# Kernel tuning notes

Hardware: AMD Instinct MI355X
Metric: run time of the kernel (lower is better)

Reference implementation:

```python
import jax, jax.numpy as jnp
import numpy as np
import math

DIM_PER_HEAD = 64

def setup_inputs() -> dict:
    key = jax.random.key(0)
    k1, k2, k3, k4 = jax.random.split(key, 4)
    B, H, S, D = 2, 16, 2048, 64
    mat1 = jax.random.normal(k1, (B, H, S, D), dtype=jnp.float32)
    mat2 = jax.random.normal(k2, (B, H, S, D), dtype=jnp.float32)
    mat3 = jax.random.normal(k3, (B, H, S, D), dtype=jnp.float32)
    bias = jax.random.normal(k4, (1, 1, S, S), dtype=jnp.float32)
    return {"mat1": mat1, "mat2": mat2, "mat3": mat3, "bias": bias}

def reference(mat1, mat2, mat3, bias) -> jnp.ndarray:
    # scale Q, scores = QK^T + bias, softmax over last dim, then @ V
    scale = 1.0 / math.sqrt(DIM_PER_HEAD)
    qk = jnp.einsum('bhqd,bhkd->bhqk', mat1 * scale, mat2)  # [B,H,S,S]
    scores = jax.nn.softmax(qk + bias, axis=-1)
    return jnp.einsum('bhqk,bhkd->bhqd', scores, mat3)
```

## Files before the change

### kernel.cpp

```cpp
#include <hip/hip_runtime.h>
#include <hip/hip_bf16.h>


#define SEQ 2048
#define DH  64
#define BHN 32
#define LOG2E 1.44269504088896f

typedef __attribute__((ext_vector_type(8))) short bf16x8;
typedef __attribute__((ext_vector_type(4))) float f32x4;
typedef __attribute__((ext_vector_type(8))) short short8v;

__device__ inline short f2b(float x) {
    union { float f; unsigned u; } v; v.f = x;
    unsigned r = v.u + 0x7fff + ((v.u >> 16) & 1);
    return (short)(r >> 16);
}

__device__ inline void gl_lds16(const void* g, void* l) {
    __builtin_amdgcn_global_load_lds(
        (const __attribute__((address_space(1))) void*)g,
        (__attribute__((address_space(3))) void*)l, 16, 0, 0);
}

__global__ __launch_bounds__(256)
void prep_kv(const float* __restrict__ K, const float* __restrict__ V,
             short* __restrict__ Kb, short* __restrict__ Vt) {
    __shared__ short t[64 * 72];
    const int tid = threadIdx.x;
    const int bh = blockIdx.x >> 5, st = blockIdx.x & 31, s0 = st * 64;

    {
        const float* Kp = K + ((size_t)bh * SEQ + s0) * DH;
        short* Ko = Kb + ((size_t)bh * SEQ + s0) * DH;
        #pragma unroll
        for (int i = 0; i < 2; ++i) {
            size_t o = (size_t)(tid + i * 256) * 8;
            f32x4 a = *(const f32x4*)(Kp + o);
            f32x4 b = *(const f32x4*)(Kp + o + 4);
            short8v s;
            #pragma unroll
            for (int j = 0; j < 4; ++j) { s[j] = f2b(a[j]); s[4 + j] = f2b(b[j]); }
            *(short8v*)(Ko + o) = s;
        }
    }

    const float* Vb = V + (size_t)bh * SEQ * DH + (size_t)s0 * DH;
    #pragma unroll
    for (int i = 0; i < 4; ++i) {
        int c = tid + i * 256, s = c >> 4, c4 = c & 15;
        f32x4 v = *(const f32x4*)(Vb + s * DH + c4 * 4);
        #pragma unroll
        for (int j = 0; j < 4; ++j) t[s * 72 + c4 * 4 + j] = f2b(v[j]);
    }
    __syncthreads();
    const int d = tid >> 2, part = tid & 3;
    short8v lo, hi;
    #pragma unroll
    for (int j = 0; j < 8; ++j) {
        lo[j] = t[(part * 16 + j) * 72 + d];
        hi[j] = t[(part * 16 + 8 + j) * 72 + d];
    }
    short* outp = Vt + (size_t)bh * DH * SEQ + (size_t)d * SEQ + s0 + part * 16;
    *(short8v*)outp = lo;
    *(short8v*)(outp + 8) = hi;
}

__global__ __launch_bounds__(256, 4)
void mha_main(const float* __restrict__ Q, const float* __restrict__ Bias,
              const short* __restrict__ Kb, const short* __restrict__ Vt,
              float* __restrict__ Out)
{
    __shared__ short lds_k[64 * DH];
    __shared__ short lds_v[DH * 64];
    __shared__ short lds_p[4 * 16 * 64];

    const int tid = threadIdx.x, lane = tid & 63, wave = tid >> 6;
    const int l15 = lane & 15, l4 = lane >> 4;
    const int qb = blockIdx.x & 31, bh = blockIdx.x >> 5;
    const int q0 = qb * 64;

    const float* Qb = Q + (size_t)bh * SEQ * DH;
    const short* Kh = Kb + (size_t)bh * SEQ * DH;
    const short* Vh = Vt + (size_t)bh * DH * SEQ;
    float* Ob = Out + (size_t)bh * SEQ * DH;

    bf16x8 qf[2];
    {
        const float* qp = Qb + (size_t)(q0 + wave * 16 + l15) * DH;
        #pragma unroll
        for (int ks = 0; ks < 2; ++ks) {
            short tmp[8];
            #pragma unroll
            for (int j = 0; j < 8; ++j) tmp[j] = f2b(qp[ks * 32 + l4 * 8 + j] * 0.125f);
            qf[ks] = *reinterpret_cast<bf16x8*>(tmp);
        }
    }

    f32x4 o_acc[4];
    #pragma unroll
    for (int dt = 0; dt < 4; ++dt) o_acc[dt] = f32x4{0.f, 0.f, 0.f, 0.f};
    float l_part[4] = {0.f, 0.f, 0.f, 0.f};

    const short* kg[2]; const short* vg[2]; short* kl[2]; short* vl[2];
    #pragma unroll
    for (int p = 0; p < 2; ++p) {
        int slot = p * 256 + wave * 64 + lane;
        int r_ = slot >> 3;
        int c_ = slot & 7;
        int cg = c_ ^ (r_ & 7);
        kg[p] = Kh + (size_t)r_ * DH + cg * 8;
        vg[p] = Vh + (size_t)r_ * SEQ + cg * 8;
        kl[p] = &lds_k[(size_t)(p * 256 + wave * 64) * 8];
        vl[p] = &lds_v[(size_t)(p * 256 + wave * 64) * 8];
    }
    const float* bp0 = Bias + (size_t)(q0 + wave * 16 + l4 * 4) * SEQ + l15;
    short* pw = &lds_p[wave * 16 * 64];
    const int swz = l15 & 7;

    for (int kt = 0; kt < SEQ / 64; ++kt) {
        const int k0 = kt * 64;
        __syncthreads();
        gl_lds16(kg[0] + (size_t)k0 * DH, kl[0]);
        gl_lds16(kg[1] + (size_t)k0 * DH, kl[1]);
        gl_lds16(vg[0] + k0, vl[0]);
        gl_lds16(vg[1] + k0, vl[1]);

        f32x4 sacc[4];
        const float* bp = bp0 + k0;
        #pragma unroll
        for (int nt = 0; nt < 4; ++nt)
            #pragma unroll
            for (int r = 0; r < 4; ++r)
                sacc[nt][r] = bp[(size_t)r * SEQ + nt * 16];

        __syncthreads();

        #pragma unroll
        for (int ks = 0; ks < 2; ++ks)
            #pragma unroll
            for (int nt = 0; nt < 4; ++nt) {
                int cc = (ks * 4 + l4) ^ swz;
                bf16x8 kf = *(const bf16x8*)&lds_k[(nt * 16 + l15) * DH + cc * 8];
                sacc[nt] = __builtin_amdgcn_mfma_f32_16x16x32_bf16(qf[ks], kf, sacc[nt], 0, 0, 0);
            }

        #pragma unroll
        for (int r = 0; r < 4; ++r) {
            const int prow = l4 * 4 + r;
            const int rsw = prow & 7;
            #pragma unroll
            for (int nt = 0; nt < 4; ++nt) {
                float pv = __builtin_amdgcn_exp2f(sacc[nt][r] * LOG2E);
                l_part[r] += pv;
                int pc = (nt * 2 + (l15 >> 3)) ^ rsw;
                pw[prow * 64 + pc * 8 + (l15 & 7)] = f2b(pv);
            }
        }

        #pragma unroll
        for (int ks = 0; ks < 2; ++ks) {
            int cc = (ks * 4 + l4) ^ swz;
            bf16x8 pf = *(const bf16x8*)&pw[l15 * 64 + cc * 8];
            #pragma unroll
            for (int dt = 0; dt < 4; ++dt) {
                bf16x8 vf = *(const bf16x8*)&lds_v[(dt * 16 + l15) * DH + cc * 8];
                o_acc[dt] = __builtin_amdgcn_mfma_f32_16x16x32_bf16(pf, vf, o_acc[dt], 0, 0, 0);
            }
        }
    }

    #pragma unroll
    for (int r = 0; r < 4; ++r) {
        float s = l_part[r];
        #pragma unroll
        for (int m = 1; m < 16; m <<= 1) s += __shfl_xor(s, m, 64);
        l_part[r] = s;
    }

    #pragma unroll
    for (int r = 0; r < 4; ++r) {
        float inv = 1.0f / l_part[r];
        float* op = Ob + (size_t)(q0 + wave * 16 + l4 * 4 + r) * DH + l15;
        #pragma unroll
        for (int dt = 0; dt < 4; ++dt) op[dt * 16] = o_acc[dt][r] * inv;
    }
}

extern "C" void kernel_launch(void* const* d_in, const int* in_sizes, int n_in,
                              void* d_out, int out_size, void* d_ws, size_t ws_size,
                              hipStream_t stream) {
    const float* Q    = (const float*)d_in[0];
    const float* K    = (const float*)d_in[1];
    const float* V    = (const float*)d_in[2];
    const float* Bias = (const float*)d_in[3];
    float* O          = (float*)d_out;

    short* Kb = (short*)d_ws;
    short* Vt = Kb + (size_t)BHN * SEQ * DH;

    prep_kv<<<dim3(BHN * 32), dim3(256), 0, stream>>>(K, V, Kb, Vt);
    mha_main<<<dim3(BHN * 32), dim3(256), 0, stream>>>(Q, Bias, Kb, Vt, O);
}
```

Measured before the change: 168.6 us.

## Double-buffer K/V tiles in LDS and prefetch bias one tile ahead

The K/V shared-memory tiles become two buffers, so the global-to-LDS load of tile kt+1 is issued while tile kt is being computed. The bias values for the next tile are also prefetched into registers. This cuts the loop to one barrier per iteration and hides global load latency behind the MFMA and exp work. LOG2E is folded into the Q scale and the bias, which removes a multiply from the exp path. In exchange, LDS use roughly doubles and register pressure rises, which could reduce occupancy.

```diff
diff --git a/kernel.cpp b/kernel.cpp
--- a/kernel.cpp
+++ b/kernel.cpp
@@ -5,6 +5,7 @@
 #define SEQ 2048
 #define DH  64
 #define BHN 32
+#define NTILE (SEQ / 64)
 #define LOG2E 1.44269504088896f
 
 typedef __attribute__((ext_vector_type(8))) short bf16x8;
@@ -71,8 +72,8 @@
               const short* __restrict__ Kb, const short* __restrict__ Vt,
               float* __restrict__ Out)
 {
-    __shared__ short lds_k[64 * DH];
-    __shared__ short lds_v[DH * 64];
+    __shared__ short lds_k[2][64 * DH];
+    __shared__ short lds_v[2][64 * DH];
     __shared__ short lds_p[4 * 16 * 64];
 
     const int tid = threadIdx.x, lane = tid & 63, wave = tid >> 6;
@@ -88,11 +89,12 @@
     bf16x8 qf[2];
     {
         const float* qp = Qb + (size_t)(q0 + wave * 16 + l15) * DH;
+        const float qs = 0.125f * LOG2E;
         #pragma unroll
         for (int ks = 0; ks < 2; ++ks) {
             short tmp[8];
             #pragma unroll
-            for (int j = 0; j < 8; ++j) tmp[j] = f2b(qp[ks * 32 + l4 * 8 + j] * 0.125f);
+            for (int j = 0; j < 8; ++j) tmp[j] = f2b(qp[ks * 32 + l4 * 8 + j] * qs);
             qf[ks] = *reinterpret_cast<bf16x8*>(tmp);
         }
     }
@@ -111,37 +113,66 @@
         int cg = c_ ^ (r_ & 7);
         kg[p] = Kh + (size_t)r_ * DH + cg * 8;
         vg[p] = Vh + (size_t)r_ * SEQ + cg * 8;
-        kl[p] = &lds_k[(size_t)(p * 256 + wave * 64) * 8];
-        vl[p] = &lds_v[(size_t)(p * 256 + wave * 64) * 8];
+        kl[p] = &lds_k[0][(size_t)(p * 256 + wave * 64) * 8];
+        vl[p] = &lds_v[0][(size_t)(p * 256 + wave * 64) * 8];
     }
     const float* bp0 = Bias + (size_t)(q0 + wave * 16 + l4 * 4) * SEQ + l15;
     short* pw = &lds_p[wave * 16 * 64];
     const int swz = l15 & 7;
 
-    for (int kt = 0; kt < SEQ / 64; ++kt) {
-        const int k0 = kt * 64;
-        __syncthreads();
-        gl_lds16(kg[0] + (size_t)k0 * DH, kl[0]);
-        gl_lds16(kg[1] + (size_t)k0 * DH, kl[1]);
-        gl_lds16(vg[0] + k0, vl[0]);
-        gl_lds16(vg[1] + k0, vl[1]);
+    gl_lds16(kg[0], kl[0]);
+    gl_lds16(kg[1], kl[1]);
+    gl_lds16(vg[0], vl[0]);
+    gl_lds16(vg[1], vl[1]);
+
+    float bpre[4][4];
+    #pragma unroll
+    for (int nt = 0; nt < 4; ++nt)
+        #pragma unroll
+        for (int r = 0; r < 4; ++r)
+            bpre[nt][r] = bp0[(size_t)r * SEQ + nt * 16];
+
+    __syncthreads();
+
+    for (int kt = 0; kt < NTILE; ++kt) {
+        const int cur = kt & 1;
+        const int nb = cur ^ 1;
+
+        if (kt + 1 < NTILE) {
+            const size_t koff = (size_t)(kt + 1) * 64 * DH;
+            const int voff = (kt + 1) * 64;
+            const int lo = nb * (64 * DH);
+            gl_lds16(kg[0] + koff, kl[0] + lo);
+            gl_lds16(kg[1] + koff, kl[1] + lo);
+            gl_lds16(vg[0] + voff, vl[0] + lo);
+            gl_lds16(vg[1] + voff, vl[1] + lo);
+        }
 
         f32x4 sacc[4];
-        const float* bp = bp0 + k0;
         #pragma unroll
         for (int nt = 0; nt < 4; ++nt)
             #pragma unroll
             for (int r = 0; r < 4; ++r)
-                sacc[nt][r] = bp[(size_t)r * SEQ + nt * 16];
-
-        __syncthreads();
+                sacc[nt][r] = bpre[nt][r] * LOG2E;
+
+        if (kt + 1 < NTILE) {
+            const float* bp = bp0 + (kt + 1) * 64;
+            #pragma unroll
+            for (int nt = 0; nt < 4; ++nt)
+                #pragma unroll
+                for (int r = 0; r < 4; ++r)
+                    bpre[nt][r] = bp[(size_t)r * SEQ + nt * 16];
+        }
+
+        const short* lk = lds_k[cur];
+        const short* lv = lds_v[cur];
 
         #pragma unroll
         for (int ks = 0; ks < 2; ++ks)
             #pragma unroll
             for (int nt = 0; nt < 4; ++nt) {
                 int cc = (ks * 4 + l4) ^ swz;
-                bf16x8 kf = *(const bf16x8*)&lds_k[(nt * 16 + l15) * DH + cc * 8];
+                bf16x8 kf = *(const bf16x8*)&lk[(nt * 16 + l15) * DH + cc * 8];
                 sacc[nt] = __builtin_amdgcn_mfma_f32_16x16x32_bf16(qf[ks], kf, sacc[nt], 0, 0, 0);
             }
 
@@ -151,7 +182,7 @@
             const int rsw = prow & 7;
             #pragma unroll
             for (int nt = 0; nt < 4; ++nt) {
-                float pv = __builtin_amdgcn_exp2f(sacc[nt][r] * LOG2E);
+                float pv = __builtin_amdgcn_exp2f(sacc[nt][r]);
                 l_part[r] += pv;
                 int pc = (nt * 2 + (l15 >> 3)) ^ rsw;
                 pw[prow * 64 + pc * 8 + (l15 & 7)] = f2b(pv);
@@ -164,10 +195,12 @@
             bf16x8 pf = *(const bf16x8*)&pw[l15 * 64 + cc * 8];
             #pragma unroll
             for (int dt = 0; dt < 4; ++dt) {
-                bf16x8 vf = *(const bf16x8*)&lds_v[(dt * 16 + l15) * DH + cc * 8];
+                bf16x8 vf = *(const bf16x8*)&lv[(dt * 16 + l15) * DH + cc * 8];
                 o_acc[dt] = __builtin_amdgcn_mfma_f32_16x16x32_bf16(pf, vf, o_acc[dt], 0, 0, 0);
             }
         }
+
+        __syncthreads();
     }
 
     #pragma unroll
```

Result: no change. 169.4 us (+0.5%).

## Keep softmax probabilities in registers via transposed MFMA and permlane swaps

Applied to the files above, without the earlier changes.

Swaps the MFMA operand order so S^T is computed, giving each lane a row's contiguous keys. The bias can then be read as float4 vectors and the P tile repacked into the PV A-operand with packed bf16 converts and permlane16/32 swaps, which drops the LDS round trip for P. LOG2E is folded into the Q scale and the bias, and the row-sum reduction becomes two shuffles plus a broadcast. It uses gfx950-specific instructions, and the correctness of the lane permutation depends on the MFMA register layout.

```diff
diff --git a/kernel.cpp b/kernel.cpp
--- a/kernel.cpp
+++ b/kernel.cpp
@@ -5,6 +5,7 @@
 #define SEQ 2048
 #define DH  64
 #define BHN 32
+#define NTILE (SEQ / 64)
 #define LOG2E 1.44269504088896f
 
 typedef __attribute__((ext_vector_type(8))) short bf16x8;
@@ -15,6 +16,19 @@
     union { float f; unsigned u; } v; v.f = x;
     unsigned r = v.u + 0x7fff + ((v.u >> 16) & 1);
     return (short)(r >> 16);
+}
+
+__device__ inline unsigned cvt_pk(float lo, float hi) {
+    unsigned r;
+    asm("v_cvt_pk_bf16_f32 %0, %1, %2" : "=v"(r) : "v"(lo), "v"(hi));
+    return r;
+}
+
+__device__ inline void pl32swap(unsigned& x, unsigned& y) {
+    asm("v_permlane32_swap_b32 %0, %1" : "+v"(x), "+v"(y));
+}
+__device__ inline void pl16swap(unsigned& x, unsigned& y) {
+    asm("v_permlane16_swap_b32 %0, %1" : "+v"(x), "+v"(y));
 }
 
 __device__ inline void gl_lds16(const void* g, void* l) {
@@ -72,13 +86,13 @@
               float* __restrict__ Out)
 {
     __shared__ short lds_k[64 * DH];
-    __shared__ short lds_v[DH * 64];
-    __shared__ short lds_p[4 * 16 * 64];
+    __shared__ short lds_v[64 * DH];
 
     const int tid = threadIdx.x, lane = tid & 63, wave = tid >> 6;
     const int l15 = lane & 15, l4 = lane >> 4;
     const int qb = blockIdx.x & 31, bh = blockIdx.x >> 5;
     const int q0 = qb * 64;
+    const int qw = q0 + wave * 16;
 
     const float* Qb = Q + (size_t)bh * SEQ * DH;
     const short* Kh = Kb + (size_t)bh * SEQ * DH;
@@ -87,12 +101,13 @@
 
     bf16x8 qf[2];
     {
-        const float* qp = Qb + (size_t)(q0 + wave * 16 + l15) * DH;
+        const float* qp = Qb + (size_t)(qw + l15) * DH;
+        const float qs = 0.125f * LOG2E;
         #pragma unroll
         for (int ks = 0; ks < 2; ++ks) {
             short tmp[8];
             #pragma unroll
-            for (int j = 0; j < 8; ++j) tmp[j] = f2b(qp[ks * 32 + l4 * 8 + j] * 0.125f);
+            for (int j = 0; j < 8; ++j) tmp[j] = f2b(qp[ks * 32 + l4 * 8 + j] * qs);
             qf[ks] = *reinterpret_cast<bf16x8*>(tmp);
         }
     }
@@ -100,7 +115,7 @@
     f32x4 o_acc[4];
     #pragma unroll
     for (int dt = 0; dt < 4; ++dt) o_acc[dt] = f32x4{0.f, 0.f, 0.f, 0.f};
-    float l_part[4] = {0.f, 0.f, 0.f, 0.f};
+    float l_acc = 0.f;
 
     const short* kg[2]; const short* vg[2]; short* kl[2]; short* vl[2];
     #pragma unroll
@@ -114,11 +129,10 @@
         kl[p] = &lds_k[(size_t)(p * 256 + wave * 64) * 8];
         vl[p] = &lds_v[(size_t)(p * 256 + wave * 64) * 8];
     }
-    const float* bp0 = Bias + (size_t)(q0 + wave * 16 + l4 * 4) * SEQ + l15;
-    short* pw = &lds_p[wave * 16 * 64];
+    const float* bp0 = Bias + (size_t)(qw + l15) * SEQ + l4 * 4;
     const int swz = l15 & 7;
 
-    for (int kt = 0; kt < SEQ / 64; ++kt) {
+    for (int kt = 0; kt < NTILE; ++kt) {
         const int k0 = kt * 64;
         __syncthreads();
         gl_lds16(kg[0] + (size_t)k0 * DH, kl[0]);
@@ -129,10 +143,11 @@
         f32x4 sacc[4];
         const float* bp = bp0 + k0;
         #pragma unroll
-        for (int nt = 0; nt < 4; ++nt)
-            #pragma unroll
-            for (int r = 0; r < 4; ++r)
-                sacc[nt][r] = bp[(size_t)r * SEQ + nt * 16];
+        for (int nt = 0; nt < 4; ++nt) {
+            f32x4 b = *(const f32x4*)(bp + nt * 16);
+            #pragma unroll
+            for (int r = 0; r < 4; ++r) sacc[nt][r] = b[r] * LOG2E;
+        }
 
         __syncthreads();
 
@@ -142,26 +157,32 @@
             for (int nt = 0; nt < 4; ++nt) {
                 int cc = (ks * 4 + l4) ^ swz;
                 bf16x8 kf = *(const bf16x8*)&lds_k[(nt * 16 + l15) * DH + cc * 8];
-                sacc[nt] = __builtin_amdgcn_mfma_f32_16x16x32_bf16(qf[ks], kf, sacc[nt], 0, 0, 0);
+                sacc[nt] = __builtin_amdgcn_mfma_f32_16x16x32_bf16(kf, qf[ks], sacc[nt], 0, 0, 0);
             }
 
-        #pragma unroll
-        for (int r = 0; r < 4; ++r) {
-            const int prow = l4 * 4 + r;
-            const int rsw = prow & 7;
-            #pragma unroll
-            for (int nt = 0; nt < 4; ++nt) {
-                float pv = __builtin_amdgcn_exp2f(sacc[nt][r] * LOG2E);
-                l_part[r] += pv;
-                int pc = (nt * 2 + (l15 >> 3)) ^ rsw;
-                pw[prow * 64 + pc * 8 + (l15 & 7)] = f2b(pv);
-            }
+        unsigned pkw[4][2];
+        #pragma unroll
+        for (int nt = 0; nt < 4; ++nt) {
+            float p0 = __builtin_amdgcn_exp2f(sacc[nt][0]);
+            float p1 = __builtin_amdgcn_exp2f(sacc[nt][1]);
+            float p2 = __builtin_amdgcn_exp2f(sacc[nt][2]);
+            float p3 = __builtin_amdgcn_exp2f(sacc[nt][3]);
+            l_acc += (p0 + p1) + (p2 + p3);
+            pkw[nt][0] = cvt_pk(p0, p1);
+            pkw[nt][1] = cvt_pk(p2, p3);
         }
 
         #pragma unroll
         for (int ks = 0; ks < 2; ++ks) {
+            unsigned A = pkw[2 * ks][0], B = pkw[2 * ks][1];
+            unsigned C = pkw[2 * ks + 1][0], D = pkw[2 * ks + 1][1];
+            pl32swap(A, C); pl16swap(A, C);
+            pl32swap(B, D); pl16swap(B, D);
+            union { unsigned w[4]; bf16x8 v; } u;
+            u.w[0] = A; u.w[1] = B; u.w[2] = C; u.w[3] = D;
+            bf16x8 pf = u.v;
+
             int cc = (ks * 4 + l4) ^ swz;
-            bf16x8 pf = *(const bf16x8*)&pw[l15 * 64 + cc * 8];
             #pragma unroll
             for (int dt = 0; dt < 4; ++dt) {
                 bf16x8 vf = *(const bf16x8*)&lds_v[(dt * 16 + l15) * DH + cc * 8];
@@ -170,18 +191,14 @@
         }
     }
 
+    l_acc += __shfl_xor(l_acc, 16, 64);
+    l_acc += __shfl_xor(l_acc, 32, 64);
+    float linv = 1.0f / l_acc;
+
     #pragma unroll
     for (int r = 0; r < 4; ++r) {
-        float s = l_part[r];
-        #pragma unroll
-        for (int m = 1; m < 16; m <<= 1) s += __shfl_xor(s, m, 64);
-        l_part[r] = s;
-    }
-
-    #pragma unroll
-    for (int r = 0; r < 4; ++r) {
-        float inv = 1.0f / l_part[r];
-        float* op = Ob + (size_t)(q0 + wave * 16 + l4 * 4 + r) * DH + l15;
+        float inv = __shfl(linv, l4 * 4 + r, 64);
+        float* op = Ob + (size_t)(qw + l4 * 4 + r) * DH + l15;
         #pragma unroll
         for (int dt = 0; dt < 4; ++dt) op[dt * 16] = o_acc[dt][r] * inv;
     }
```

Result: slower. 181.6 us (+7.7%).

## Double KV tile to 128 and swizzle block order for L2 locality

Applied to the files above, without the earlier changes.

Raises the K/V tile loaded per iteration from 64 to 128 keys, so each loop does two 64-key halves of QK, exp and PV between a single pair of barriers, halving the barrier and loop-overhead count. The second half's bias is loaded inside the loop after the first half's compute. Block indices are also remapped so that consecutive blocks are spread across heads, which is meant to change L2 sharing of the bias and K/V streams. LDS use grows, which may reduce occupancy. The P buffer is reused between halves with no barrier, relying on per-wave ordering.

```diff
diff --git a/kernel.cpp b/kernel.cpp
--- a/kernel.cpp
+++ b/kernel.cpp
@@ -5,6 +5,8 @@
 #define SEQ 2048
 #define DH  64
 #define BHN 32
+#define KV  128
+#define NTILE (SEQ / KV)
 #define LOG2E 1.44269504088896f
 
 typedef __attribute__((ext_vector_type(8))) short bf16x8;
@@ -71,13 +73,16 @@
               const short* __restrict__ Kb, const short* __restrict__ Vt,
               float* __restrict__ Out)
 {
-    __shared__ short lds_k[64 * DH];
-    __shared__ short lds_v[DH * 64];
+    __shared__ short lds_k[KV * DH];
+    __shared__ short lds_v[DH * KV];
     __shared__ short lds_p[4 * 16 * 64];
 
     const int tid = threadIdx.x, lane = tid & 63, wave = tid >> 6;
     const int l15 = lane & 15, l4 = lane >> 4;
-    const int qb = blockIdx.x & 31, bh = blockIdx.x >> 5;
+
+    const int bid = blockIdx.x;
+    const int swzb = (bid & 7) * (BHN * 32 / 8) + (bid >> 3);
+    const int qb = swzb & 31, bh = swzb >> 5;
     const int q0 = qb * 64;
 
     const float* Qb = Q + (size_t)bh * SEQ * DH;
@@ -102,70 +107,90 @@
     for (int dt = 0; dt < 4; ++dt) o_acc[dt] = f32x4{0.f, 0.f, 0.f, 0.f};
     float l_part[4] = {0.f, 0.f, 0.f, 0.f};
 
-    const short* kg[2]; const short* vg[2]; short* kl[2]; short* vl[2];
-    #pragma unroll
-    for (int p = 0; p < 2; ++p) {
-        int slot = p * 256 + wave * 64 + lane;
-        int r_ = slot >> 3;
-        int c_ = slot & 7;
-        int cg = c_ ^ (r_ & 7);
-        kg[p] = Kh + (size_t)r_ * DH + cg * 8;
-        vg[p] = Vh + (size_t)r_ * SEQ + cg * 8;
-        kl[p] = &lds_k[(size_t)(p * 256 + wave * 64) * 8];
-        vl[p] = &lds_v[(size_t)(p * 256 + wave * 64) * 8];
+    const short* kg[4]; const short* vg[4]; short* kl[4]; short* vl[4];
+    #pragma unroll
+    for (int p = 0; p < 4; ++p) {
+        int slot = p * 256 + tid;
+        int kr = slot >> 3, kc = slot & 7;
+        int kcg = kc ^ (kr & 7);
+        kg[p] = Kh + (size_t)kr * DH + kcg * 8;
+        kl[p] = &lds_k[(size_t)slot * 8];
+        int vr = slot >> 4, vc = slot & 15;
+        int vcg = vc ^ (vr & 7);
+        vg[p] = Vh + (size_t)vr * SEQ + vcg * 8;
+        vl[p] = &lds_v[(size_t)slot * 8];
     }
     const float* bp0 = Bias + (size_t)(q0 + wave * 16 + l4 * 4) * SEQ + l15;
     short* pw = &lds_p[wave * 16 * 64];
     const int swz = l15 & 7;
 
-    for (int kt = 0; kt < SEQ / 64; ++kt) {
-        const int k0 = kt * 64;
+    for (int kt = 0; kt < NTILE; ++kt) {
+        const int k0 = kt * KV;
         __syncthreads();
-        gl_lds16(kg[0] + (size_t)k0 * DH, kl[0]);
-        gl_lds16(kg[1] + (size_t)k0 * DH, kl[1]);
-        gl_lds16(vg[0] + k0, vl[0]);
-        gl_lds16(vg[1] + k0, vl[1]);
+        #pragma unroll
+        for (int p = 0; p < 4; ++p) {
+            gl_lds16(kg[p] + (size_t)k0 * DH, kl[p]);
+            gl_lds16(vg[p] + k0, vl[p]);
+        }
 
         f32x4 sacc[4];
-        const float* bp = bp0 + k0;
-        #pragma unroll
-        for (int nt = 0; nt < 4; ++nt)
-            #pragma unroll
-            for (int r = 0; r < 4; ++r)
-                sacc[nt][r] = bp[(size_t)r * SEQ + nt * 16];
+        {
+            const float* bp = bp0 + k0;
+            #pragma unroll
+            for (int nt = 0; nt < 4; ++nt)
+                #pragma unroll
+                for (int r = 0; r < 4; ++r)
+                    sacc[nt][r] = bp[(size_t)r * SEQ + nt * 16];
+        }
 
         __syncthreads();
 
         #pragma unroll
-        for (int ks = 0; ks < 2; ++ks)
-            #pragma unroll
-            for (int nt = 0; nt < 4; ++nt) {
+        for (int hh = 0; hh < 2; ++hh) {
+            if (hh) {
+                const float* bp = bp0 + k0 + 64;
+                #pragma unroll
+                for (int nt = 0; nt < 4; ++nt)
+                    #pragma unroll
+                    for (int r = 0; r < 4; ++r)
+                        sacc[nt][r] = bp[(size_t)r * SEQ + nt * 16];
+            }
+
+            #pragma unroll
+            for (int ks = 0; ks < 2; ++ks)
+                #pragma unroll
+                for (int nt = 0; nt < 4; ++nt) {
+                    int cc = (ks * 4 + l4) ^ swz;
+                    bf16x8 kf = *(const bf16x8*)
+                        &lds_k[(hh * 64 + nt * 16 + l15) * DH + cc * 8];
+                    sacc[nt] = __builtin_amdgcn_mfma_f32_16x16x32_bf16(
+                        qf[ks], kf, sacc[nt], 0, 0, 0);
+                }
+
+            #pragma unroll
+            for (int r = 0; r < 4; ++r) {
+                const int prow = l4 * 4 + r;
+                const int rsw = prow & 7;
+                #pragma unroll
+                for (int nt = 0; nt < 4; ++nt) {
+                    float pv = __builtin_amdgcn_exp2f(sacc[nt][r] * LOG2E);
+                    l_part[r] += pv;
+                    int pc = (nt * 2 + (l15 >> 3)) ^ rsw;
+                    pw[prow * 64 + pc * 8 + (l15 & 7)] = f2b(pv);
+                }
+            }
+
+            #pragma unroll
+            for (int ks = 0; ks < 2; ++ks) {
                 int cc = (ks * 4 + l4) ^ swz;
-                bf16x8 kf = *(const bf16x8*)&lds_k[(nt * 16 + l15) * DH + cc * 8];
-                sacc[nt] = __builtin_amdgcn_mfma_f32_16x16x32_bf16(qf[ks], kf, sacc[nt], 0, 0, 0);
-            }
-
-        #pragma unroll
-        for (int r = 0; r < 4; ++r) {
-            const int prow = l4 * 4 + r;
-            const int rsw = prow & 7;
-            #pragma unroll
-            for (int nt = 0; nt < 4; ++nt) {
-                float pv = __builtin_amdgcn_exp2f(sacc[nt][r] * LOG2E);
-                l_part[r] += pv;
-                int pc = (nt * 2 + (l15 >> 3)) ^ rsw;
-                pw[prow * 64 + pc * 8 + (l15 & 7)] = f2b(pv);
-            }
-        }
-
-        #pragma unroll
-        for (int ks = 0; ks < 2; ++ks) {
-            int cc = (ks * 4 + l4) ^ swz;
-            bf16x8 pf = *(const bf16x8*)&pw[l15 * 64 + cc * 8];
-            #pragma unroll
-            for (int dt = 0; dt < 4; ++dt) {
-                bf16x8 vf = *(const bf16x8*)&lds_v[(dt * 16 + l15) * DH + cc * 8];
-                o_acc[dt] = __builtin_amdgcn_mfma_f32_16x16x32_bf16(pf, vf, o_acc[dt], 0, 0, 0);
+                bf16x8 pf = *(const bf16x8*)&pw[l15 * 64 + cc * 8];
+                #pragma unroll
+                for (int dt = 0; dt < 4; ++dt) {
+                    bf16x8 vf = *(const bf16x8*)
+                        &lds_v[(dt * 16 + l15) * KV + (hh * 8 + cc) * 8];
+                    o_acc[dt] = __builtin_amdgcn_mfma_f32_16x16x32_bf16(
+                        pf, vf, o_acc[dt], 0, 0, 0);
+                }
             }
         }
     }
```

Result: slower. 172.1 us (+2.1%).
